# Optimization experiments

Hardware: AMD Instinct MI355X
Metric: run time of the kernel (lower is better)

Reference implementation:

```python
import jax, jax.numpy as jnp
import numpy as np

B_SZ, N, NX, NU, NY, NW = 128, 2048, 64, 32, 64, 64


def setup_inputs() -> dict:
    key = jax.random.key(0)
    ks = jax.random.split(key, 10)
    sx = 1.0 / np.sqrt(NX)
    su = 1.0 / np.sqrt(NU)
    sw = 1.0 / np.sqrt(NW)
    return {
        "x0": jax.random.normal(ks[0], (B_SZ, NX), jnp.float32),
        "us": jax.random.normal(ks[1], (B_SZ, N, NU), jnp.float32),
        # state matrix scaled for (approximate) stability of the recurrence
        "A": 0.9 * sx * jax.random.normal(ks[2], (NX, NX), jnp.float32),
        "B1": su * jax.random.normal(ks[3], (NX, NU), jnp.float32),
        "B2": sw * jax.random.normal(ks[4], (NX, NW), jnp.float32),
        "C1": sx * jax.random.normal(ks[5], (NY, NX), jnp.float32),
        "D11": su * jax.random.normal(ks[6], (NY, NU), jnp.float32),
        "D12": sw * jax.random.normal(ks[7], (NY, NW), jnp.float32),
        "C2": sx * jax.random.normal(ks[8], (NW, NX), jnp.float32),
        "D21": su * jax.random.normal(ks[9], (NW, NU), jnp.float32),
    }


def reference(x0, us, A, B1, B2, C1, D11, D12, C2, D21):
    """LureSystem.forward: sequential Lure recurrence with tanh nonlinearity.

    x0: [B, nx], us: [B, N, nu] -> ys: [B, N, ny]
    Per step k (matching torch: x is updated BEFORE computing y_k):
      w = tanh(C2 x + D21 u_k)
      x <- A x + B1 u_k + B2 w
      y_k = C1 x + D11 u_k + D12 w
    """
    def step(x, u):
        w = jnp.tanh(x @ C2.T + u @ D21.T)          # [B, nw]
        x_next = x @ A.T + u @ B1.T + w @ B2.T      # [B, nx]
        y = x_next @ C1.T + u @ D11.T + w @ D12.T   # [B, ny]
        return x_next, y

    us_t = jnp.swapaxes(us, 0, 1)                    # [N, B, nu]
    _, ys_t = jax.lax.scan(step, x0, us_t)           # ys_t: [N, B, ny]
    return jnp.swapaxes(ys_t, 0, 1)                  # [B, N, ny]
```

## Files before the change

### kernel.cpp

```cpp
#include <hip/hip_runtime.h>


#define NT 2048

typedef __attribute__((ext_vector_type(8))) short short8;
typedef __attribute__((ext_vector_type(4))) float f4;
typedef __attribute__((ext_vector_type(2))) int i2;

union Frag { int i[4]; i2 h[2]; short8 v; };

__device__ __forceinline__ unsigned rne_bf16(float f) {
  unsigned u = __float_as_uint(f);
  return (u + 0x7FFFu + ((u >> 16) & 1u)) >> 16;
}
__device__ __forceinline__ void split2(float a, float b, int& hi, int& lo) {
  unsigned ha = rne_bf16(a), hb = rne_bf16(b);
  float ra = a - __uint_as_float(ha << 16);
  float rb = b - __uint_as_float(hb << 16);
  hi = (int)(ha | (hb << 16));
  lo = (int)(rne_bf16(ra) | (rne_bf16(rb) << 16));
}
__device__ __forceinline__ void split8(const float* x, Frag& hi, Frag& lo) {
#pragma unroll
  for (int p = 0; p < 4; p++) split2(x[2 * p], x[2 * p + 1], hi.i[p], lo.i[p]);
}
__device__ __forceinline__ int cvtpk(float a, float b) {
  int r;
  asm("v_cvt_pk_bf16_f32 %0, %1, %2" : "=v"(r) : "v"(a), "v"(b));
  return r;
}
__device__ __forceinline__ void split2c(float a, float b, int& hi, int& lo) {
  hi = cvtpk(a, b);
  float ra = a - __uint_as_float((unsigned)hi << 16);
  float rb = b - __uint_as_float((unsigned)hi & 0xFFFF0000u);
  lo = cvtpk(ra, rb);
}
__device__ __forceinline__ float ftanh(float x) {
  float e = __expf(2.0f * x);
  return 1.0f - 2.0f * __builtin_amdgcn_rcpf(e + 1.0f);
}
__device__ __forceinline__ f4 mf(const Frag& a, const Frag& b, f4 c) {
  return __builtin_amdgcn_mfma_f32_16x16x32_bf16(a.v, b.v, c, 0, 0, 0);
}
__device__ __forceinline__ float ror8f(float x) {
  return __int_as_float(
      __builtin_amdgcn_mov_dpp(__float_as_int(x), 0x128, 0xf, 0xf, true));
}
__device__ __forceinline__ void lds_barrier() {
  __builtin_amdgcn_s_waitcnt(0xC07F);
  __builtin_amdgcn_s_barrier();
}
__device__ __forceinline__ void wfrag(const float* W, int row0, int c, int lane,
                                      Frag& hi, Frag& lo) {
  const int m = lane & 15, qq = lane >> 4;
  const f4* p = (const f4*)(W + (size_t)(row0 + m) * 192 + 32 * c + 8 * qq);
  f4 a = p[0], b = p[1];
  float t[8] = {a[0], a[1], a[2], a[3], b[0], b[1], b[2], b[3]};
  split8(t, hi, lo);
}

__global__ void prep_w(const float* __restrict__ A, const float* __restrict__ B1,
                       const float* __restrict__ B2, const float* __restrict__ C1,
                       const float* __restrict__ D11, const float* __restrict__ D12,
                       const float* __restrict__ C2, const float* __restrict__ D21,
                       float* __restrict__ Wfull) {
  const int r = blockIdx.x;
  const int c = threadIdx.x;
  float v = 0.f;
  if (c < 64) {
    const int j = c;
    if (r < 64) v = A[r * 64 + j];
    else if (r < 128) { float s = 0.f; for (int l = 0; l < 64; l++) s += C2[(r - 64) * 64 + l] * A[l * 64 + j]; v = s; }
    else { float s = 0.f; for (int l = 0; l < 64; l++) s += C1[(r - 128) * 64 + l] * A[l * 64 + j]; v = s; }
  } else if (c < 128) {
    const int j = c - 64;
    if (r < 64) v = B2[r * 64 + j];
    else if (r < 128) { float s = 0.f; for (int l = 0; l < 64; l++) s += C2[(r - 64) * 64 + l] * B2[l * 64 + j]; v = s; }
    else { float s = 0.f; for (int l = 0; l < 64; l++) s += C1[(r - 128) * 64 + l] * B2[l * 64 + j]; v = s + D12[(r - 128) * 64 + j]; }
  } else if (c < 160) {
    const int j = c - 128;
    if (r < 64) v = B1[r * 32 + j];
    else if (r < 128) { float s = 0.f; for (int l = 0; l < 64; l++) s += C2[(r - 64) * 64 + l] * B1[l * 32 + j]; v = s; }
    else { float s = 0.f; for (int l = 0; l < 64; l++) s += C1[(r - 128) * 64 + l] * B1[l * 32 + j]; v = s + D11[(r - 128) * 32 + j]; }
  } else {
    const int j = c - 160;
    v = (r >= 64 && r < 128) ? D21[(r - 64) * 32 + j] : 0.f;
  }
  Wfull[r * 192 + c] = v;
}

__global__ __launch_bounds__(256)
void prep_uu(const float* __restrict__ us, const float* __restrict__ Wfull,
             float* __restrict__ UU) {
  const int blk = blockIdx.x;
  const int kc = blockIdx.y;
  const int wv = threadIdx.x >> 6;
  const int lane = threadIdx.x & 63;
  const int nn = lane & 15, q = lane >> 4;
  const int b0 = blk * 16;

  Frag zh4, zl4, zh5, zl5, xh4, xl4, yh4, yl4;
  wfrag(Wfull, 64 + 16 * wv, 4, lane, zh4, zl4);
  wfrag(Wfull, 64 + 16 * wv, 5, lane, zh5, zl5);
  wfrag(Wfull, 16 * wv, 4, lane, xh4, xl4);
  wfrag(Wfull, 128 + 16 * wv, 4, lane, yh4, yl4);

  const float* ubase = us + (size_t)(b0 + nn) * (NT * 32) + 8 * q;

  int k = kc * 32;
  Frag uhc, ulc, uhn, uln;
  {
    const f4* p = (const f4*)(ubase + (size_t)k * 32);
    f4 a = p[0], b = p[1];
    float t[8] = {a[0], a[1], a[2], a[3], b[0], b[1], b[2], b[3]};
    split8(t, uhc, ulc);
  }
  f4 ra, rb;
  {
    const int kn = (k + 1 < NT) ? k + 1 : NT - 1;
    const f4* p = (const f4*)(ubase + (size_t)kn * 32);
    ra = p[0]; rb = p[1];
  }
  for (int k0 = 0; k0 < 32; k0++, k++) {
    {
      float t[8] = {ra[0], ra[1], ra[2], ra[3], rb[0], rb[1], rb[2], rb[3]};
      split8(t, uhn, uln);
    }
    {
      const int kp = (k + 2 < NT) ? k + 2 : NT - 1;
      const f4* p = (const f4*)(ubase + (size_t)kp * 32);
      ra = p[0]; rb = p[1];
    }
    f4 az = {0.f, 0.f, 0.f, 0.f}, ax = az, ay = az;
    az = mf(zh4, uhc, az); az = mf(zh5, uhn, az);
    az = mf(zh4, ulc, az); az = mf(zh5, uln, az);
    az = mf(zl4, uhc, az); az = mf(zl5, uhn, az);
    ax = mf(xh4, uhc, ax); ax = mf(xh4, ulc, ax); ax = mf(xl4, uhc, ax);
    ay = mf(yh4, uhc, ay); ay = mf(yh4, ulc, ay); ay = mf(yl4, uhc, ay);
    float* dst = UU + ((size_t)k * 8 + blk) * 3072 + lane * 4;
    *(f4*)(dst + wv * 256) = az;
    *(f4*)(dst + (4 + wv) * 256) = ax;
    *(f4*)(dst + (8 + wv) * 256) = ay;
    uhc = uhn; ulc = uln;
  }
}

__global__ __launch_bounds__(512, 1)
void lure_seqp(const float* __restrict__ x0, const float* __restrict__ us,
               const float* __restrict__ C2, const float* __restrict__ D21,
               const float* __restrict__ Wfull, const float* __restrict__ UU,
               float* __restrict__ out) {
  __shared__ int lds[2][4][272];
  const int tid = threadIdx.x;
  const int wave = tid >> 6;
  const int lane = tid & 63;
  const int q = lane >> 4;
  const int nn = lane & 15;
  const int b8 = blockIdx.x * 8;
  const int ro = q * 68 + nn * 4;
  const size_t KSTRIDE = 8 * 12 * 256;
  const int ob = blockIdx.x >> 1, hh = blockIdx.x & 1;
  const int ulane = 8 * hh + (lane & 7) + 16 * q;
  const float msk = (lane & 8) ? 0.f : 1.f;

  if (tid < 128) {
    const int n = tid >> 4;
    const int f0 = (tid & 15) * 4;
    const int c = f0 >> 5;
    const int g = (f0 & 31) >> 3;
    const int d = (f0 & 7) >> 1;
    const int idx = g * 68 + n * 4 + d;
    const float* xrow = x0 + (b8 + n) * 64;
    float xv[4] = {xrow[f0], xrow[f0 + 1], xrow[f0 + 2], xrow[f0 + 3]};
    int h0, l0, h1, l1;
    split2(xv[0], xv[1], h0, l0);
    split2(xv[2], xv[3], h1, l1);
    lds[0][c][idx] = h0;       lds[0][c][idx + 1] = h1;
    lds[0][c][idx + 32] = l0;  lds[0][c][idx + 33] = l1;
    float zv[4] = {0.f, 0.f, 0.f, 0.f};
    for (int j = 0; j < 64; j++) {
      float xj = xrow[j];
#pragma unroll
      for (int r = 0; r < 4; r++) zv[r] += C2[(f0 + r) * 64 + j] * xj;
    }
    const float* urow = us + (size_t)(b8 + n) * (NT * 32);
    for (int j = 0; j < 32; j++) {
      float uj = urow[j];
#pragma unroll
      for (int r = 0; r < 4; r++) zv[r] += D21[(f0 + r) * 32 + j] * uj;
    }
#pragma unroll
    for (int r = 0; r < 4; r++) zv[r] = ftanh(zv[r]);
    split2(zv[0], zv[1], h0, l0);
    split2(zv[2], zv[3], h1, l1);
    lds[0][2 + c][idx] = h0;       lds[0][2 + c][idx + 1] = h1;
    lds[0][2 + c][idx + 32] = l0;  lds[0][2 + c][idx + 33] = l1;
  }

  if (wave < 4) {
    const int zt = wave;
    Frag WH[4], WL[4];
#pragma unroll
    for (int c = 0; c < 4; c++) wfrag(Wfull, 64 + 16 * zt, c, lane, WH[c], WL[c]);
    const float* up = UU + (((size_t)ob * 12 + zt) * 64 + ulane) * 4;
    f4 uz[4];
#pragma unroll
    for (int d = 0; d < 4; d++) uz[d] = *(const f4*)(up + (size_t)d * KSTRIDE);
    const int widx = (2 * (zt & 1) + (q >> 1)) * 68 + nn * 4 + 2 * (q & 1);
    const int rw = 2 + (zt >> 1);
    lds_barrier();

    auto zstep = [&](int kk, int d, int kp) {
      const int rb = kk & 1;
      Frag b[4];
#pragma unroll
      for (int c = 0; c < 4; c++) b[c].v = *(const short8*)&lds[rb][c][ro];
      f4 sA0 = {uz[d][0] * msk, uz[d][1] * msk, uz[d][2] * msk, uz[d][3] * msk};
      f4 z4 = {0.f, 0.f, 0.f, 0.f};
      f4 sA1 = z4, sB0 = z4, sB1 = z4;
      sA0 = mf(WH[0], b[0], sA0); sB0 = mf(WL[0], b[0], sB0);
      sA1 = mf(WH[1], b[1], sA1); sB1 = mf(WL[1], b[1], sB1);
      sA0 = mf(WH[2], b[2], sA0); sB0 = mf(WL[2], b[2], sB0);
      sA1 = mf(WH[3], b[3], sA1); sB1 = mf(WL[3], b[3], sB1);
      uz[d] = *(const f4*)(up + (size_t)kp * KSTRIDE);
      float wv[4];
#pragma unroll
      for (int r = 0; r < 4; r++) {
        float aa = sA0[r] + sA1[r];
        wv[r] = ftanh(aa + ror8f(aa) + (sB0[r] + sB1[r]));
      }
      int h0, l0, h1, l1;
      split2c(wv[0], wv[1], h0, l0);
      split2c(wv[2], wv[3], h1, l1);
      if ((lane & 8) == 0) {
        i2 wh; wh[0] = h0; wh[1] = h1;
        i2 wl; wl[0] = l0; wl[1] = l1;
        *(i2*)&lds[rb ^ 1][rw][widx] = wh;
        *(i2*)&lds[rb ^ 1][rw][widx + 32] = wl;
      }
      lds_barrier();
    };
    int k = 0;
    for (; k < NT - 4; k += 4) {
      zstep(k, 0, k + 4); zstep(k + 1, 1, k + 5);
      zstep(k + 2, 2, k + 6); zstep(k + 3, 3, k + 7);
    }
    zstep(k, 0, NT - 1); zstep(k + 1, 1, NT - 1);
    zstep(k + 2, 2, NT - 1); zstep(k + 3, 3, NT - 1);
  } else {
    const int xt = wave - 4;
    Frag WXH[4], WXL[4], WYH[4];
#pragma unroll
    for (int c = 0; c < 4; c++) {
      wfrag(Wfull, 16 * xt, c, lane, WXH[c], WXL[c]);
      Frag dmy;
      wfrag(Wfull, 128 + 16 * xt, c, lane, WYH[c], dmy);
    }
    const float* upx = UU + (((size_t)ob * 12 + 4 + xt) * 64 + ulane) * 4;
    const float* upy = UU + (((size_t)ob * 12 + 8 + xt) * 64 + ulane) * 4;
    f4 ux[4], uy[4];
#pragma unroll
    for (int d = 0; d < 4; d++) {
      ux[d] = *(const f4*)(upx + (size_t)d * KSTRIDE);
      uy[d] = *(const f4*)(upy + (size_t)d * KSTRIDE);
    }
    const int widx = (2 * (xt & 1) + (q >> 1)) * 68 + nn * 4 + 2 * (q & 1);
    const int rw = (xt >> 1);
    float* py0 = out + (size_t)(b8 + nn) * (NT * 64) + 16 * xt + 4 * q;
    lds_barrier();

    auto xstep = [&](int kk, int d, int kp) {
      const int rb = kk & 1;
      Frag b[4];
#pragma unroll
      for (int c = 0; c < 4; c++) b[c].v = *(const short8*)&lds[rb][c][ro];
      f4 tA0 = {ux[d][0] * msk, ux[d][1] * msk, ux[d][2] * msk, ux[d][3] * msk};
      f4 z4 = {0.f, 0.f, 0.f, 0.f};
      f4 tA1 = z4, tB0 = z4, tB1 = z4;
      f4 sy = uy[d];
      tA0 = mf(WXH[0], b[0], tA0); tB0 = mf(WXL[0], b[0], tB0);
      tA1 = mf(WXH[1], b[1], tA1); tB1 = mf(WXL[1], b[1], tB1);
      sy = mf(WYH[0], b[0], sy);   sy = mf(WYH[1], b[1], sy);
      tA0 = mf(WXH[2], b[2], tA0); tB0 = mf(WXL[2], b[2], tB0);
      tA1 = mf(WXH[3], b[3], tA1); tB1 = mf(WXL[3], b[3], tB1);
      sy = mf(WYH[2], b[2], sy);   sy = mf(WYH[3], b[3], sy);
      ux[d] = *(const f4*)(upx + (size_t)kp * KSTRIDE);
      uy[d] = *(const f4*)(upy + (size_t)kp * KSTRIDE);
      float xv[4];
#pragma unroll
      for (int r = 0; r < 4; r++) {
        float aa = tA0[r] + tA1[r];
        xv[r] = aa + ror8f(aa) + (tB0[r] + tB1[r]);
      }
      int h0, l0, h1, l1;
      split2c(xv[0], xv[1], h0, l0);
      split2c(xv[2], xv[3], h1, l1);
      if ((lane & 8) == 0) {
        i2 wh; wh[0] = h0; wh[1] = h1;
        i2 wl; wl[0] = l0; wl[1] = l1;
        *(i2*)&lds[rb ^ 1][rw][widx] = wh;
        *(i2*)&lds[rb ^ 1][rw][widx + 32] = wl;
        *(f4*)(py0 + (size_t)kk * 64) = sy;
      }
      lds_barrier();
    };
    int k = 0;
    for (; k < NT - 4; k += 4) {
      xstep(k, 0, k + 4); xstep(k + 1, 1, k + 5);
      xstep(k + 2, 2, k + 6); xstep(k + 3, 3, k + 7);
    }
    xstep(k, 0, NT - 1); xstep(k + 1, 1, NT - 1);
    xstep(k + 2, 2, NT - 1); xstep(k + 3, 3, NT - 1);
  }
}

__global__ __launch_bounds__(256, 1)
void lure_seq_fb(const float* __restrict__ x0, const float* __restrict__ us,
                 const float* __restrict__ C2, const float* __restrict__ D21,
                 const float* __restrict__ Wfull, float* __restrict__ out) {
  __shared__ int lds[2][8][272];
  const int tid = threadIdx.x;
  const int wave = tid >> 6;
  const int lane = tid & 63;
  const int q = lane >> 4;
  const int nn = lane & 15;
  const int b0 = blockIdx.x * 16;
  const int ro = q * 68 + nn * 4;
  {
    const int n = tid >> 4;
    const int f0 = (tid & 15) * 4;
    const int cc = f0 >> 5;
    const int g = (f0 & 31) >> 3;
    const int d = (f0 & 7) >> 1;
    const int idx = g * 68 + n * 4 + d;
    const float* xrow = x0 + (b0 + n) * 64;
    float xv[4] = {xrow[f0], xrow[f0 + 1], xrow[f0 + 2], xrow[f0 + 3]};
    int h0, l0, h1, l1;
    split2(xv[0], xv[1], h0, l0);
    split2(xv[2], xv[3], h1, l1);
    lds[0][cc][idx] = h0;     lds[0][cc][idx + 1] = h1;
    lds[0][2 + cc][idx] = l0; lds[0][2 + cc][idx + 1] = l1;
    float zv[4] = {0.f, 0.f, 0.f, 0.f};
    for (int j = 0; j < 64; j++) {
      float xj = xrow[j];
#pragma unroll
      for (int r = 0; r < 4; r++) zv[r] += C2[(f0 + r) * 64 + j] * xj;
    }
    const float* urow = us + (size_t)(b0 + n) * (NT * 32);
    for (int j = 0; j < 32; j++) {
      float uj = urow[j];
#pragma unroll
      for (int r = 0; r < 4; r++) zv[r] += D21[(f0 + r) * 32 + j] * uj;
    }
#pragma unroll
    for (int r = 0; r < 4; r++) zv[r] = ftanh(zv[r]);
    split2(zv[0], zv[1], h0, l0);
    split2(zv[2], zv[3], h1, l1);
    lds[0][4 + cc][idx] = h0; lds[0][4 + cc][idx + 1] = h1;
    lds[0][6 + cc][idx] = l0; lds[0][6 + cc][idx + 1] = l1;
  }
  Frag uh[2], ul[2];
  f4 ra0[4], ra1[4];
  const float* pu = us + ((size_t)(b0 + nn) * NT) * 32 + 8 * q;
#pragma unroll
  for (int j = 0; j < 2; j++) {
    const f4* p = (const f4*)(pu + j * 32);
    f4 a = p[0], b = p[1];
    float t[8] = {a[0], a[1], a[2], a[3], b[0], b[1], b[2], b[3]};
    split8(t, uh[j], ul[j]);
  }
#pragma unroll
  for (int j = 2; j <= 5; j++) {
    const f4* p = (const f4*)(pu + j * 32);
    ra0[j & 3] = p[0];
    ra1[j & 3] = p[1];
  }
  lds_barrier();

  if (wave < 2) {
    const int Z0 = wave * 2;
    Frag WH[2][6], WL[2][6];
#pragma unroll
    for (int t = 0; t < 2; t++)
#pragma unroll
      for (int c = 0; c < 6; c++)
        wfrag(Wfull, 64 + 16 * (Z0 + t), c, lane, WH[t][c], WL[t][c]);
    auto zstep = [&](int kk, int uu) {
      const int rb = uu & 1;
      Frag bh[4], bl[4];
#pragma unroll
      for (int c = 0; c < 4; c++) {
        const int s = (c < 2) ? c : 2 + c;
        bh[c].v = *(const short8*)&lds[rb][s][ro];
        bl[c].v = *(const short8*)&lds[rb][s + 2][ro];
      }
      const int i4 = uu & 1, i5 = (uu + 1) & 1;
#pragma unroll
      for (int t = 0; t < 2; t++) {
        f4 z4 = {0.f, 0.f, 0.f, 0.f};
        f4 s1a = z4, s1b = z4, s2a = z4, s2b = z4, s3a = z4, s3b = z4;
        s1a = mf(WH[t][0], bh[0], s1a); s1b = mf(WH[t][1], bh[1], s1b);
        s2a = mf(WH[t][0], bl[0], s2a); s2b = mf(WH[t][1], bl[1], s2b);
        s3a = mf(WL[t][0], bh[0], s3a); s3b = mf(WL[t][1], bh[1], s3b);
        s1a = mf(WH[t][2], bh[2], s1a); s1b = mf(WH[t][3], bh[3], s1b);
        s2a = mf(WH[t][2], bl[2], s2a); s2b = mf(WH[t][3], bl[3], s2b);
        s3a = mf(WL[t][2], bh[2], s3a); s3b = mf(WL[t][3], bh[3], s3b);
        s1a = mf(WH[t][4], uh[i4], s1a); s1b = mf(WH[t][5], uh[i5], s1b);
        s2a = mf(WH[t][4], ul[i4], s2a); s2b = mf(WH[t][5], ul[i5], s2b);
        s3a = mf(WL[t][4], uh[i4], s3a); s3b = mf(WL[t][5], uh[i5], s3b);
        float wv[4];
#pragma unroll
        for (int r = 0; r < 4; r++)
          wv[r] = ftanh(((s1a[r] + s1b[r]) + (s2a[r] + s2b[r])) + (s3a[r] + s3b[r]));
        int h0, l0, h1, l1;
        split2(wv[0], wv[1], h0, l0);
        split2(wv[2], wv[3], h1, l1);
        const int zt = Z0 + t;
        const int widx = (2 * (zt & 1) + (q >> 1)) * 68 + nn * 4 + 2 * (q & 1);
        i2 wh; wh[0] = h0; wh[1] = h1;
        i2 wl; wl[0] = l0; wl[1] = l1;
        *(i2*)&lds[rb ^ 1][4 + (zt >> 1)][widx] = wh;
        *(i2*)&lds[rb ^ 1][6 + (zt >> 1)][widx] = wl;
      }
      f4 a = ra0[(uu + 2) & 3], b = ra1[(uu + 2) & 3];
      float t8[8] = {a[0], a[1], a[2], a[3], b[0], b[1], b[2], b[3]};
      split8(t8, uh[uu & 1], ul[uu & 1]);
      const int kp = (kk + 6 < NT) ? kk + 6 : NT - 1;
      const f4* p = (const f4*)(pu + (size_t)kp * 32);
      ra0[(uu + 2) & 3] = p[0];
      ra1[(uu + 2) & 3] = p[1];
      lds_barrier();
    };
    for (int k = 0; k < NT; k += 4) {
      zstep(k, 0); zstep(k + 1, 1); zstep(k + 2, 2); zstep(k + 3, 3);
    }
  } else {
    const int X0 = (wave - 2) * 2;
    Frag WXH[2][5], WXL[2][5], WYH[2][5];
#pragma unroll
    for (int t = 0; t < 2; t++)
#pragma unroll
      for (int c = 0; c < 5; c++) {
        wfrag(Wfull, 16 * (X0 + t), c, lane, WXH[t][c], WXL[t][c]);
        Frag dmy;
        wfrag(Wfull, 128 + 16 * (X0 + t), c, lane, WYH[t][c], dmy);
      }
    float* py0 = out + (size_t)(b0 + nn) * (NT * 64) + 16 * X0 + 4 * q;
    auto xstep = [&](int kk, int uu) {
      const int rb = uu & 1;
      Frag bh[4], bl[4];
#pragma unroll
      for (int c = 0; c < 4; c++) {
        const int s = (c < 2) ? c : 2 + c;
        bh[c].v = *(const short8*)&lds[rb][s][ro];
        bl[c].v = *(const short8*)&lds[rb][s + 2][ro];
      }
      const int i4 = uu & 1;
#pragma unroll
      for (int t = 0; t < 2; t++) {
        f4 z4 = {0.f, 0.f, 0.f, 0.f};
        f4 s1 = z4, s2 = z4, s3 = z4, sy = z4;
#pragma unroll
        for (int c = 0; c < 4; c++) {
          s1 = mf(WXH[t][c], bh[c], s1);
          s2 = mf(WXH[t][c], bl[c], s2);
          s3 = mf(WXL[t][c], bh[c], s3);
          sy = mf(WYH[t][c], bh[c], sy);
        }
        s1 = mf(WXH[t][4], uh[i4], s1);
        s2 = mf(WXH[t][4], ul[i4], s2);
        s3 = mf(WXL[t][4], uh[i4], s3);
        sy = mf(WYH[t][4], uh[i4], sy);
        float xv[4];
#pragma unroll
        for (int r = 0; r < 4; r++) xv[r] = s1[r] + s2[r] + s3[r];
        int h0, l0, h1, l1;
        split2(xv[0], xv[1], h0, l0);
        split2(xv[2], xv[3], h1, l1);
        const int xt = X0 + t;
        const int widx = (2 * (xt & 1) + (q >> 1)) * 68 + nn * 4 + 2 * (q & 1);
        i2 wh; wh[0] = h0; wh[1] = h1;
        i2 wl; wl[0] = l0; wl[1] = l1;
        *(i2*)&lds[rb ^ 1][(xt >> 1)][widx] = wh;
        *(i2*)&lds[rb ^ 1][2 + (xt >> 1)][widx] = wl;
        *(f4*)(py0 + (size_t)kk * 64 + 16 * t) = sy;
      }
      f4 a = ra0[(uu + 2) & 3], b = ra1[(uu + 2) & 3];
      float t8[8] = {a[0], a[1], a[2], a[3], b[0], b[1], b[2], b[3]};
      split8(t8, uh[uu & 1], ul[uu & 1]);
      const int kp = (kk + 6 < NT) ? kk + 6 : NT - 1;
      const f4* p = (const f4*)(pu + (size_t)kp * 32);
      ra0[(uu + 2) & 3] = p[0];
      ra1[(uu + 2) & 3] = p[1];
      lds_barrier();
    };
    for (int k = 0; k < NT; k += 4) {
      xstep(k, 0); xstep(k + 1, 1); xstep(k + 2, 2); xstep(k + 3, 3);
    }
  }
}

extern "C" void kernel_launch(void* const* d_in, const int* in_sizes, int n_in,
                              void* d_out, int out_size, void* d_ws, size_t ws_size,
                              hipStream_t stream) {
  const float* x0  = (const float*)d_in[0];
  const float* us  = (const float*)d_in[1];
  const float* A   = (const float*)d_in[2];
  const float* B1  = (const float*)d_in[3];
  const float* B2  = (const float*)d_in[4];
  const float* C1  = (const float*)d_in[5];
  const float* D11 = (const float*)d_in[6];
  const float* D12 = (const float*)d_in[7];
  const float* C2  = (const float*)d_in[8];
  const float* D21 = (const float*)d_in[9];
  float* Wfull = (float*)d_ws;
  const size_t W_BYTES = (size_t)192 * 192 * 4;
  float* UU = (float*)((char*)d_ws + W_BYTES);
  const size_t UU_BYTES = (size_t)NT * 8 * 12 * 256 * 4;
  const bool pre = ws_size >= W_BYTES + UU_BYTES;
  float* out = (float*)d_out;

  prep_w<<<dim3(192), dim3(192), 0, stream>>>(A, B1, B2, C1, D11, D12, C2, D21, Wfull);
  if (pre) {
    prep_uu<<<dim3(8, 64), dim3(256), 0, stream>>>(us, Wfull, UU);
    lure_seqp<<<dim3(16), dim3(512), 0, stream>>>(x0, us, C2, D21, Wfull, UU, out);
  } else {
    lure_seq_fb<<<dim3(8), dim3(256), 0, stream>>>(x0, us, C2, D21, Wfull, out);
  }
}
```

Baseline: 983.7 us.

## Split z-recurrence with lookahead term to shorten critical dependency chain

Adds a second precomputed weight matrix (C2A·A, C2A·B2, etc.) so the z-waves compute next-step pre-activation contributions one step ahead, carried in a register (pz). The critical path per step now uses only two MFMAs on the w-fragments plus the precomputed init, while the lookahead MFMAs run off the critical chain. The u-dependent projection in prep_uu grows to three time taps. This adds more MFMAs per step and an extra prep kernel, and it changes rounding behaviour through the composed weights.

```diff
diff --git a/kernel.cpp b/kernel.cpp
--- a/kernel.cpp
+++ b/kernel.cpp
@@ -50,13 +50,17 @@
   __builtin_amdgcn_s_waitcnt(0xC07F);
   __builtin_amdgcn_s_barrier();
 }
-__device__ __forceinline__ void wfrag(const float* W, int row0, int c, int lane,
-                                      Frag& hi, Frag& lo) {
+__device__ __forceinline__ void wfragS(const float* W, int stride, int row0, int c,
+                                       int lane, Frag& hi, Frag& lo) {
   const int m = lane & 15, qq = lane >> 4;
-  const f4* p = (const f4*)(W + (size_t)(row0 + m) * 192 + 32 * c + 8 * qq);
+  const f4* p = (const f4*)(W + (size_t)(row0 + m) * stride + 32 * c + 8 * qq);
   f4 a = p[0], b = p[1];
   float t[8] = {a[0], a[1], a[2], a[3], b[0], b[1], b[2], b[3]};
   split8(t, hi, lo);
+}
+__device__ __forceinline__ void wfrag(const float* W, int row0, int c, int lane,
+                                      Frag& hi, Frag& lo) {
+  wfragS(W, 192, row0, c, lane, hi, lo);
 }
 
 __global__ void prep_w(const float* __restrict__ A, const float* __restrict__ B1,
@@ -89,9 +93,25 @@
   Wfull[r * 192 + c] = v;
 }
 
+__global__ void prep_w2(const float* __restrict__ A, const float* __restrict__ B1,
+                        const float* __restrict__ B2, const float* __restrict__ D21,
+                        const float* __restrict__ Wfull, float* __restrict__ W2) {
+  const int r = blockIdx.x;
+  const int c = threadIdx.x;
+  const float* c2a = Wfull + (size_t)(64 + r) * 192;
+  float v = 0.f;
+  if (c < 64) { float s = 0.f; for (int l = 0; l < 64; l++) s += c2a[l] * A[l * 64 + c]; v = s; }
+  else if (c < 128) { float s = 0.f; for (int l = 0; l < 64; l++) s += c2a[l] * B2[l * 64 + (c - 64)]; v = s; }
+  else if (c < 192) { v = c2a[64 + (c - 128)]; }
+  else if (c < 224) { float s = 0.f; for (int l = 0; l < 64; l++) s += c2a[l] * B1[l * 32 + (c - 192)]; v = s; }
+  else if (c < 256) { v = c2a[128 + (c - 224)]; }
+  else { v = D21[r * 32 + (c - 256)]; }
+  W2[(size_t)r * 288 + c] = v;
+}
+
 __global__ __launch_bounds__(256)
 void prep_uu(const float* __restrict__ us, const float* __restrict__ Wfull,
-             float* __restrict__ UU) {
+             const float* __restrict__ W2, float* __restrict__ UU) {
   const int blk = blockIdx.x;
   const int kc = blockIdx.y;
   const int wv = threadIdx.x >> 6;
@@ -99,16 +119,26 @@
   const int nn = lane & 15, q = lane >> 4;
   const int b0 = blk * 16;
 
-  Frag zh4, zl4, zh5, zl5, xh4, xl4, yh4, yl4;
-  wfrag(Wfull, 64 + 16 * wv, 4, lane, zh4, zl4);
-  wfrag(Wfull, 64 + 16 * wv, 5, lane, zh5, zl5);
+  Frag zh6, zl6, zh7, zl7, zh8, zl8, xh4, xl4, yh4, yl4;
+  wfragS(W2, 288, 16 * wv, 6, lane, zh6, zl6);
+  wfragS(W2, 288, 16 * wv, 7, lane, zh7, zl7);
+  wfragS(W2, 288, 16 * wv, 8, lane, zh8, zl8);
   wfrag(Wfull, 16 * wv, 4, lane, xh4, xl4);
   wfrag(Wfull, 128 + 16 * wv, 4, lane, yh4, yl4);
 
   const float* ubase = us + (size_t)(b0 + nn) * (NT * 32) + 8 * q;
 
   int k = kc * 32;
-  Frag uhc, ulc, uhn, uln;
+  Frag uhp, ulp, uhc, ulc, uhn, uln;
+  if (kc == 0) {
+#pragma unroll
+    for (int p = 0; p < 4; p++) { uhp.i[p] = 0; ulp.i[p] = 0; }
+  } else {
+    const f4* p = (const f4*)(ubase + (size_t)(k - 1) * 32);
+    f4 a = p[0], b = p[1];
+    float t[8] = {a[0], a[1], a[2], a[3], b[0], b[1], b[2], b[3]};
+    split8(t, uhp, ulp);
+  }
   {
     const f4* p = (const f4*)(ubase + (size_t)k * 32);
     f4 a = p[0], b = p[1];
@@ -132,15 +162,16 @@
       ra = p[0]; rb = p[1];
     }
     f4 az = {0.f, 0.f, 0.f, 0.f}, ax = az, ay = az;
-    az = mf(zh4, uhc, az); az = mf(zh5, uhn, az);
-    az = mf(zh4, ulc, az); az = mf(zh5, uln, az);
-    az = mf(zl4, uhc, az); az = mf(zl5, uhn, az);
+    az = mf(zh6, uhp, az); az = mf(zh7, uhc, az); az = mf(zh8, uhn, az);
+    az = mf(zh6, ulp, az); az = mf(zh7, ulc, az); az = mf(zh8, uln, az);
+    az = mf(zl6, uhp, az); az = mf(zl7, uhc, az); az = mf(zl8, uhn, az);
     ax = mf(xh4, uhc, ax); ax = mf(xh4, ulc, ax); ax = mf(xl4, uhc, ax);
     ay = mf(yh4, uhc, ay); ay = mf(yh4, ulc, ay); ay = mf(yl4, uhc, ay);
     float* dst = UU + ((size_t)k * 8 + blk) * 3072 + lane * 4;
     *(f4*)(dst + wv * 256) = az;
     *(f4*)(dst + (4 + wv) * 256) = ax;
     *(f4*)(dst + (8 + wv) * 256) = ay;
+    uhp = uhc; ulp = ulc;
     uhc = uhn; ulc = uln;
   }
 }
@@ -148,8 +179,8 @@
 __global__ __launch_bounds__(512, 1)
 void lure_seqp(const float* __restrict__ x0, const float* __restrict__ us,
                const float* __restrict__ C2, const float* __restrict__ D21,
-               const float* __restrict__ Wfull, const float* __restrict__ UU,
-               float* __restrict__ out) {
+               const float* __restrict__ Wfull, const float* __restrict__ W2,
+               const float* __restrict__ UU, float* __restrict__ out) {
   __shared__ int lds[2][4][272];
   const int tid = threadIdx.x;
   const int wave = tid >> 6;
@@ -199,29 +230,50 @@
 
   if (wave < 4) {
     const int zt = wave;
-    Frag WH[4], WL[4];
-#pragma unroll
-    for (int c = 0; c < 4; c++) wfrag(Wfull, 64 + 16 * zt, c, lane, WH[c], WL[c]);
+    Frag QH[2], QL[2], PH[4], PL[4];
+#pragma unroll
+    for (int c = 0; c < 2; c++) wfragS(W2, 288, 16 * zt, 4 + c, lane, QH[c], QL[c]);
+#pragma unroll
+    for (int c = 0; c < 4; c++) wfragS(W2, 288, 16 * zt, c, lane, PH[c], PL[c]);
     const float* up = UU + (((size_t)ob * 12 + zt) * 64 + ulane) * 4;
     f4 uz[4];
 #pragma unroll
     for (int d = 0; d < 4; d++) uz[d] = *(const f4*)(up + (size_t)d * KSTRIDE);
+    f4 pz;
+    {
+      const int bb = lane & 7;
+      const float* xrow = x0 + (size_t)(b8 + bb) * 64;
+      const float* wr = Wfull + (size_t)(64 + 16 * zt + 4 * q) * 192;
+      float acc[4] = {0.f, 0.f, 0.f, 0.f};
+      for (int j = 0; j < 64; j++) {
+        float xj = xrow[j];
+#pragma unroll
+        for (int r = 0; r < 4; r++) acc[r] += wr[r * 192 + j] * xj;
+      }
+      pz[0] = acc[0]; pz[1] = acc[1]; pz[2] = acc[2]; pz[3] = acc[3];
+    }
     const int widx = (2 * (zt & 1) + (q >> 1)) * 68 + nn * 4 + 2 * (q & 1);
     const int rw = 2 + (zt >> 1);
     lds_barrier();
 
     auto zstep = [&](int kk, int d, int kp) {
       const int rb = kk & 1;
-      Frag b[4];
-#pragma unroll
-      for (int c = 0; c < 4; c++) b[c].v = *(const short8*)&lds[rb][c][ro];
-      f4 sA0 = {uz[d][0] * msk, uz[d][1] * msk, uz[d][2] * msk, uz[d][3] * msk};
+      Frag bw0, bw1, bx0, bx1;
+      bw0.v = *(const short8*)&lds[rb][2][ro];
+      bw1.v = *(const short8*)&lds[rb][3][ro];
+      bx0.v = *(const short8*)&lds[rb][0][ro];
+      bx1.v = *(const short8*)&lds[rb][1][ro];
+      f4 init = {(uz[d][0] + pz[0]) * msk, (uz[d][1] + pz[1]) * msk,
+                 (uz[d][2] + pz[2]) * msk, (uz[d][3] + pz[3]) * msk};
       f4 z4 = {0.f, 0.f, 0.f, 0.f};
-      f4 sA1 = z4, sB0 = z4, sB1 = z4;
-      sA0 = mf(WH[0], b[0], sA0); sB0 = mf(WL[0], b[0], sB0);
-      sA1 = mf(WH[1], b[1], sA1); sB1 = mf(WL[1], b[1], sB1);
-      sA0 = mf(WH[2], b[2], sA0); sB0 = mf(WL[2], b[2], sB0);
-      sA1 = mf(WH[3], b[3], sA1); sB1 = mf(WL[3], b[3], sB1);
+      f4 sA0 = mf(QH[0], bw0, init);
+      f4 sA1 = mf(QH[1], bw1, z4);
+      f4 sB0 = mf(QL[0], bw0, z4);
+      f4 sB1 = mf(QL[1], bw1, z4);
+      f4 pA0 = mf(PH[2], bw0, mf(PH[0], bx0, z4));
+      f4 pA1 = mf(PH[3], bw1, mf(PH[1], bx1, z4));
+      f4 pB0 = mf(PL[2], bw0, mf(PL[0], bx0, z4));
+      f4 pB1 = mf(PL[3], bw1, mf(PL[1], bx1, z4));
       uz[d] = *(const f4*)(up + (size_t)kp * KSTRIDE);
       float wv[4];
 #pragma unroll
@@ -237,6 +289,11 @@
         i2 wl; wl[0] = l0; wl[1] = l1;
         *(i2*)&lds[rb ^ 1][rw][widx] = wh;
         *(i2*)&lds[rb ^ 1][rw][widx + 32] = wl;
+      }
+#pragma unroll
+      for (int r = 0; r < 4; r++) {
+        float pa = pA0[r] + pA1[r];
+        pz[r] = pa + ror8f(pa) + (pB0[r] + pB1[r]);
       }
       lds_barrier();
     };
@@ -515,15 +572,18 @@
   const float* D21 = (const float*)d_in[9];
   float* Wfull = (float*)d_ws;
   const size_t W_BYTES = (size_t)192 * 192 * 4;
-  float* UU = (float*)((char*)d_ws + W_BYTES);
+  float* W2 = (float*)((char*)d_ws + W_BYTES);
+  const size_t W2_BYTES = (size_t)64 * 288 * 4;
+  float* UU = (float*)((char*)d_ws + W_BYTES + W2_BYTES);
   const size_t UU_BYTES = (size_t)NT * 8 * 12 * 256 * 4;
-  const bool pre = ws_size >= W_BYTES + UU_BYTES;
+  const bool pre = ws_size >= W_BYTES + W2_BYTES + UU_BYTES;
   float* out = (float*)d_out;
 
   prep_w<<<dim3(192), dim3(192), 0, stream>>>(A, B1, B2, C1, D11, D12, C2, D21, Wfull);
   if (pre) {
-    prep_uu<<<dim3(8, 64), dim3(256), 0, stream>>>(us, Wfull, UU);
-    lure_seqp<<<dim3(16), dim3(512), 0, stream>>>(x0, us, C2, D21, Wfull, UU, out);
+    prep_w2<<<dim3(64), dim3(288), 0, stream>>>(A, B1, B2, D21, Wfull, W2);
+    prep_uu<<<dim3(8, 64), dim3(256), 0, stream>>>(us, Wfull, W2, UU);
+    lure_seqp<<<dim3(16), dim3(512), 0, stream>>>(x0, us, C2, D21, Wfull, W2, UU, out);
   } else {
     lure_seq_fb<<<dim3(8), dim3(256), 0, stream>>>(x0, us, C2, D21, Wfull, out);
   }
```

Result: slower. 1.011 ms (+2.8%).

## Fuse UU precompute into sequential kernel with atomic completion flag

Applied to the files above, without the earlier changes.

Merges the prep_uu work into the main recurrence kernel by adding extra producer blocks that compute the UU tiles, while the 16 sequential blocks do their init and then spin on an atomic counter before starting the recurrence. This removes a separate kernel launch boundary and overlaps the sequential blocks' setup with UU production. It adds a memset and relies on all blocks being co-resident to avoid deadlock.

```diff
diff --git a/kernel.cpp b/kernel.cpp
--- a/kernel.cpp
+++ b/kernel.cpp
@@ -106,7 +106,6 @@
   wfrag(Wfull, 128 + 16 * wv, 4, lane, yh4, yl4);
 
   const float* ubase = us + (size_t)(b0 + nn) * (NT * 32) + 8 * q;
-
   int k = kc * 32;
   Frag uhc, ulc, uhn, uln;
   {
@@ -146,12 +145,74 @@
 }
 
 __global__ __launch_bounds__(512, 1)
-void lure_seqp(const float* __restrict__ x0, const float* __restrict__ us,
-               const float* __restrict__ C2, const float* __restrict__ D21,
-               const float* __restrict__ Wfull, const float* __restrict__ UU,
-               float* __restrict__ out) {
+void lure_fused(const float* __restrict__ x0, const float* __restrict__ us,
+                const float* __restrict__ C2, const float* __restrict__ D21,
+                const float* __restrict__ Wfull, float* __restrict__ UU,
+                float* __restrict__ out, unsigned* done) {
   __shared__ int lds[2][4][272];
   const int tid = threadIdx.x;
+
+  if (blockIdx.x >= 16) {
+    const int stride = (gridDim.x - 16) * 2;
+    const int unit = (blockIdx.x - 16) * 2 + (tid >> 8);
+    const int t2 = tid & 255;
+    const int wv = t2 >> 6;
+    const int lane = t2 & 63;
+    const int nn = lane & 15, q = lane >> 4;
+
+    Frag zh4, zl4, zh5, zl5, xh4, xl4, yh4, yl4;
+    wfrag(Wfull, 64 + 16 * wv, 4, lane, zh4, zl4);
+    wfrag(Wfull, 64 + 16 * wv, 5, lane, zh5, zl5);
+    wfrag(Wfull, 16 * wv, 4, lane, xh4, xl4);
+    wfrag(Wfull, 128 + 16 * wv, 4, lane, yh4, yl4);
+
+    for (int tile = unit; tile < 512; tile += stride) {
+      const int blk = tile & 7, kc = tile >> 3;
+      const int b0 = blk * 16;
+      const float* ubase = us + (size_t)(b0 + nn) * (NT * 32) + 8 * q;
+      int k = kc * 32;
+      Frag uhc, ulc, uhn, uln;
+      {
+        const f4* p = (const f4*)(ubase + (size_t)k * 32);
+        f4 a = p[0], b = p[1];
+        float tt[8] = {a[0], a[1], a[2], a[3], b[0], b[1], b[2], b[3]};
+        split8(tt, uhc, ulc);
+      }
+      f4 ra, rb;
+      {
+        const int kn = (k + 1 < NT) ? k + 1 : NT - 1;
+        const f4* p = (const f4*)(ubase + (size_t)kn * 32);
+        ra = p[0]; rb = p[1];
+      }
+      for (int k0 = 0; k0 < 32; k0++, k++) {
+        {
+          float tt[8] = {ra[0], ra[1], ra[2], ra[3], rb[0], rb[1], rb[2], rb[3]};
+          split8(tt, uhn, uln);
+        }
+        {
+          const int kp = (k + 2 < NT) ? k + 2 : NT - 1;
+          const f4* p = (const f4*)(ubase + (size_t)kp * 32);
+          ra = p[0]; rb = p[1];
+        }
+        f4 az = {0.f, 0.f, 0.f, 0.f}, ax = az, ay = az;
+        az = mf(zh4, uhc, az); az = mf(zh5, uhn, az);
+        az = mf(zh4, ulc, az); az = mf(zh5, uln, az);
+        az = mf(zl4, uhc, az); az = mf(zl5, uhn, az);
+        ax = mf(xh4, uhc, ax); ax = mf(xh4, ulc, ax); ax = mf(xl4, uhc, ax);
+        ay = mf(yh4, uhc, ay); ay = mf(yh4, ulc, ay); ay = mf(yl4, uhc, ay);
+        float* dst = UU + ((size_t)k * 8 + blk) * 3072 + lane * 4;
+        *(f4*)(dst + wv * 256) = az;
+        *(f4*)(dst + (4 + wv) * 256) = ax;
+        *(f4*)(dst + (8 + wv) * 256) = ay;
+        uhc = uhn; ulc = uln;
+      }
+    }
+    __syncthreads();
+    __threadfence();
+    if (done && tid == 0) atomicAdd(done, 1u);
+    return;
+  }
+
   const int wave = tid >> 6;
   const int lane = tid & 63;
   const int q = lane >> 4;
@@ -195,6 +256,16 @@
     split2(zv[2], zv[3], h1, l1);
     lds[0][2 + c][idx] = h0;       lds[0][2 + c][idx + 1] = h1;
     lds[0][2 + c][idx + 32] = l0;  lds[0][2 + c][idx + 33] = l1;
+  }
+
+  if (done != nullptr) {
+    if (tid == 0) {
+      const unsigned target = (unsigned)(gridDim.x - 16);
+      while (__hip_atomic_load(done, __ATOMIC_ACQUIRE,
+                               __HIP_MEMORY_SCOPE_AGENT) < target)
+        __builtin_amdgcn_s_sleep(32);
+    }
+    __syncthreads();
   }
 
   if (wave < 4) {
@@ -517,13 +588,18 @@
   const size_t W_BYTES = (size_t)192 * 192 * 4;
   float* UU = (float*)((char*)d_ws + W_BYTES);
   const size_t UU_BYTES = (size_t)NT * 8 * 12 * 256 * 4;
-  const bool pre = ws_size >= W_BYTES + UU_BYTES;
+  unsigned* flag = (unsigned*)((char*)d_ws + W_BYTES + UU_BYTES);
   float* out = (float*)d_out;
 
   prep_w<<<dim3(192), dim3(192), 0, stream>>>(A, B1, B2, C1, D11, D12, C2, D21, Wfull);
-  if (pre) {
+  if (ws_size >= W_BYTES + UU_BYTES + 256) {
+    hipMemsetAsync(flag, 0, 256, stream);
+    lure_fused<<<dim3(256), dim3(512), 0, stream>>>(x0, us, C2, D21, Wfull, UU,
+                                                    out, flag);
+  } else if (ws_size >= W_BYTES + UU_BYTES) {
     prep_uu<<<dim3(8, 64), dim3(256), 0, stream>>>(us, Wfull, UU);
-    lure_seqp<<<dim3(16), dim3(512), 0, stream>>>(x0, us, C2, D21, Wfull, UU, out);
+    lure_fused<<<dim3(16), dim3(512), 0, stream>>>(x0, us, C2, D21, Wfull, UU,
+                                                   out, nullptr);
   } else {
     lure_seq_fb<<<dim3(8), dim3(256), 0, stream>>>(x0, us, C2, D21, Wfull, out);
   }
```

New measurement: 1.058 ms. 7.6% more time.
